# Kernel tuning notes

Hardware: AMD Instinct MI355X
Metric: run time of the kernel (lower is better)

## Reference

```python
import jax, jax.numpy as jnp
import numpy as np

BN_EPS = 1e-5

# Binary activation with hardtanh STE semantics (forward: sign)
@jax.custom_vjp
def binary_act(x):
    return jnp.sign(x)

def _ba_fwd(x):
    return jnp.sign(x), x

def _ba_bwd(x, g):
    return (jnp.where(jnp.abs(x) > 1.0, 0.0, g),)

binary_act.defvjp(_ba_fwd, _ba_bwd)

# Binary weight quantizer (forward: sign, backward: identity STE)
@jax.custom_vjp
def binary_w(x):
    return jnp.sign(x)

def _bw_fwd(x):
    return jnp.sign(x), None

def _bw_bwd(_, g):
    return (g,)

binary_w.defvjp(_bw_fwd, _bw_bwd)


def setup_inputs() -> dict:
    key = jax.random.key(0)
    k1, k2, k3 = jax.random.split(key, 3)
    B, C_in, H, W_sp = 32, 256, 56, 56
    C_out, KH, KW = 256, 3, 3
    x = jax.random.normal(k1, (B, C_in, H, W_sp), dtype=jnp.float32)
    weight = jax.random.normal(k2, (C_out, C_in, KH, KW), dtype=jnp.float32) * 0.05
    bias = jax.random.normal(k3, (C_out,), dtype=jnp.float32) * 0.01
    gamma = jnp.ones((C_out,), dtype=jnp.float32)
    beta = jnp.zeros((C_out,), dtype=jnp.float32)
    return {"x": x, "weight": weight, "bias": bias, "gamma": gamma, "beta": beta}


def reference(x, weight, bias, gamma, beta):
    # --- activation binarization (A=2): sign ---
    xb = binary_act(x)
    # --- weight binarization (W=2): mean-center over in-channel dim, clamp, sign * alpha ---
    wc = weight - jnp.mean(weight, axis=1, keepdims=True)
    wc = jnp.clip(wc, -1.0, 1.0)
    alpha = jnp.mean(jnp.abs(wc), axis=(1, 2, 3), keepdims=True)  # per-output-channel scale
    wq = binary_w(wc) * alpha
    # --- conv2d, stride 1, padding 1 ---
    y = jax.lax.conv_general_dilated(
        xb, wq, window_strides=(1, 1), padding=((1, 1), (1, 1)),
        dimension_numbers=("NCHW", "OIHW", "NCHW"))
    y = y + bias[None, :, None, None]
    # --- BatchNorm2d (training-mode batch statistics, biased variance) ---
    mu = jnp.mean(y, axis=(0, 2, 3), keepdims=True)
    var = jnp.var(y, axis=(0, 2, 3), keepdims=True)
    y = (y - mu) * jax.lax.rsqrt(var + BN_EPS)
    y = y * gamma[None, :, None, None] + beta[None, :, None, None]
    # --- last_relu=1 ---
    y = jax.nn.relu(y)
    # --- last_bin=1 (A=2 -> binary activation) ---
    y = binary_act(y)
    return y
```

## Files before the change

kernel.cpp:

```cpp
#include <hip/hip_runtime.h>

typedef unsigned long long u64;
typedef int i32x4 __attribute__((ext_vector_type(4)));
typedef int i32x16 __attribute__((ext_vector_type(16)));

#define N_SP 3136
#define C_IN 256
#define C_OUT 256
#define BATCH 32
#define NBLK 896
#define XROW 64
#define XPLANE (58 * XROW * 256)
#define XSIZE ((size_t)BATCH * XPLANE)

__global__ __launch_bounds__(256) void prep_weights(const float* __restrict__ w,
                                                    char* __restrict__ A_pack,
                                                    double* __restrict__ alpha) {
    const int o = blockIdx.x;
    const int i = threadIdx.x;
    const int lane = i & 63, wvid = i >> 6;
    __shared__ double part[4][9];
    __shared__ double part2[4];

    float wv[9];
    const float* wp = w + ((size_t)o * C_IN + i) * 9;
#pragma unroll
    for (int t = 0; t < 9; ++t) wv[t] = wp[t];

#pragma unroll
    for (int t = 0; t < 9; ++t) {
        double v = (double)wv[t];
#pragma unroll
        for (int off = 32; off > 0; off >>= 1) v += __shfl_down(v, off);
        if (lane == 0) part[wvid][t] = v;
    }
    __syncthreads();

    double asum = 0.0;
#pragma unroll
    for (int t = 0; t < 9; ++t) {
        double mean = (part[0][t] + part[1][t] + part[2][t] + part[3][t]) * (1.0 / 256.0);
        double wc = (double)wv[t] - mean;
        int idx16 = ((t * 8 + (i >> 5)) * 8 + (o >> 5)) * 64 + (((i >> 4) & 1) << 5) + (o & 31);
        A_pack[(size_t)idx16 * 16 + (i & 15)] = (char)(wc > 0.0 ? 1 : -1);
        double aw = fabs(wc);
        if (aw > 1.0) aw = 1.0;
        asum += aw;
    }
#pragma unroll
    for (int off = 32; off > 0; off >>= 1) asum += __shfl_down(asum, off);
    if (lane == 0) part2[wvid] = asum;
    __syncthreads();
    if (i == 0)
        alpha[o] = (part2[0] + part2[1] + part2[2] + part2[3]) * (1.0 / 2304.0);
}

__global__ __launch_bounds__(256) void zero_borders(char* __restrict__ xsT) {
    const int tid = blockIdx.x * 256 + threadIdx.x;
    const int b = tid / 9216;
    const int r = tid - b * 9216;
    int hp, wp, c16;
    if (r < 2048) {
        hp = (r >> 10) * 57;
        wp = (r >> 4) & 63;
        c16 = (r & 15) << 4;
    } else {
        int r2 = r - 2048;
        hp = 1 + (r2 >> 7);
        int q = r2 & 127;
        int wi = q >> 4;
        wp = (wi == 0) ? 0 : 56 + wi;
        c16 = (q & 15) << 4;
    }
    *(i32x4*)(xsT + (((size_t)(b * 58 + hp) << 6) + wp) * 256 + c16) = (i32x4){0, 0, 0, 0};
}

__global__ __launch_bounds__(256) void sign_transpose(const float* __restrict__ x,
                                                      char* __restrict__ xsT) {
    const int sp0 = blockIdx.x * 64;
    const int b = blockIdx.y;
    const int lane = threadIdx.x & 63;
    const int wv = threadIdx.x >> 6;
    __shared__ char tile[64 * 272];

    const float* xp = x + ((size_t)(b * 256 + (wv << 6))) * N_SP + sp0 + lane;
#pragma unroll
    for (int q = 0; q < 4; ++q) {
        unsigned d[4];
#pragma unroll
        for (int dd = 0; dd < 4; ++dd) {
            unsigned v = 0;
#pragma unroll
            for (int kk = 0; kk < 4; ++kk) {
                int ci_l = (q << 4) + (dd << 2) + kk;
                float xv = xp[(size_t)ci_l * N_SP];
                v |= (unsigned)(xv > 0.0f ? 0x01u : 0xFFu) << (8 * kk);
            }
            d[dd] = v;
        }
        *(i32x4*)(tile + lane * 272 + (wv << 6) + (q << 4)) =
            (i32x4){(int)d[0], (int)d[1], (int)d[2], (int)d[3]};
    }
    __syncthreads();

    const int t = threadIdx.x;
#pragma unroll
    for (int j = 0; j < 4; ++j) {
        int sp_loc = (j << 4) + (t >> 4);
        int ci0 = (t & 15) << 4;
        i32x4 v = *(const i32x4*)(tile + sp_loc * 272 + ci0);
        int spg = sp0 + sp_loc;
        int h = spg / 56, w = spg - h * 56;
        size_t dst = (((size_t)(b * 58 + h + 1) << 6) + (w + 1)) * 256 + ci0;
        *(i32x4*)(xsT + dst) = v;
    }
}

__global__ __launch_bounds__(256, 2) void conv_mfma(const char* __restrict__ xsT,
                                                    const char* __restrict__ A_pack,
                                                    float* __restrict__ out,
                                                    int2* __restrict__ partials) {
    const int tid = threadIdx.x;
    const int lane = tid & 63;
    const int wv = tid >> 6;
    const int l31 = lane & 31, l5 = lane >> 5;
    const int blk = blockIdx.x;
    const int y = blockIdx.y;
    const int b = blk / 28;
    const int h0 = (blk - b * 28) * 2;
    const int co5 = y * 4 + wv;

    __shared__ char slab[4 * 66 * 272];

    {
        const char* src = xsT + ((size_t)(b * 58 + h0) << 6) * 256;
        for (int c = tid; c < 4 * 64 * 16; c += 256) {
            int dh = c >> 10, rem = c & 1023, wp = rem >> 4, c16 = (rem & 15) << 4;
            *(i32x4*)(slab + (dh * 66 + wp) * 272 + c16) =
                *(const i32x4*)(src + (size_t)dh * (XROW * 256) + wp * 256 + c16);
        }
        if (tid < 128) {
            int dh = tid >> 5, wp = 64 + ((tid >> 4) & 1), c16 = (tid & 15) << 4;
            *(i32x4*)(slab + (dh * 66 + wp) * 272 + c16) = (i32x4){0, 0, 0, 0};
        }
    }
    __syncthreads();

    i32x16 acc[2][2] = {};

#pragma unroll
    for (int tap = 0; tap < 9; ++tap) {
        const int dh = tap / 3, dw = tap % 3;
#pragma unroll
        for (int cib = 0; cib < 8; ++cib) {
            i32x4 af = *(const i32x4*)(A_pack +
                ((size_t)(((tap * 8 + cib) * 8 + co5) * 64 + lane) << 4));
            i32x4 bf[2][2];
#pragma unroll
            for (int nh = 0; nh < 2; ++nh)
#pragma unroll
                for (int row = 0; row < 2; ++row)
                    bf[nh][row] = *(const i32x4*)(slab +
                        ((dh + row) * 66 + (nh * 32 + l31) + dw) * 272 + l5 * 16 + cib * 32);
#pragma unroll
            for (int nh = 0; nh < 2; ++nh)
#pragma unroll
                for (int row = 0; row < 2; ++row)
                    acc[nh][row] = __builtin_amdgcn_mfma_i32_32x32x32_i8(
                        af, bf[nh][row], acc[nh][row], 0, 0, 0);
        }
    }

    float* ob = out + ((size_t)(b * 256 + co5 * 32)) * N_SP + h0 * 56;
#pragma unroll
    for (int nh = 0; nh < 2; ++nh) {
        const int w = nh * 32 + l31;
        if (w < 56) {
#pragma unroll
            for (int row = 0; row < 2; ++row)
#pragma unroll
                for (int reg = 0; reg < 16; ++reg) {
                    int corow = (reg & 3) + 8 * (reg >> 2) + 4 * l5;
                    ob[(size_t)corow * N_SP + row * 56 + w] = (float)acc[nh][row][reg];
                }
        }
    }

    __syncthreads();
    int* sp_s = (int*)slab;
    int* sp_q = (int*)slab + 128;
#pragma unroll
    for (int reg = 0; reg < 16; ++reg) {
        int v00 = acc[0][0][reg], v01 = acc[0][1][reg];
        int v10 = (l31 < 24) ? acc[1][0][reg] : 0;
        int v11 = (l31 < 24) ? acc[1][1][reg] : 0;
        int s = v00 + v01 + v10 + v11;
        unsigned q = (unsigned)(v00 * v00) + (unsigned)(v01 * v01)
                   + (unsigned)(v10 * v10) + (unsigned)(v11 * v11);
#pragma unroll
        for (int off = 16; off > 0; off >>= 1) {
            s += __shfl_xor(s, off);
            q += (unsigned)__shfl_xor((int)q, off);
        }
        if (l31 == 0) {
            int corow = (reg & 3) + 8 * (reg >> 2) + 4 * l5;
            sp_s[wv * 32 + corow] = s;
            sp_q[wv * 32 + corow] = (int)q;
        }
    }
    __syncthreads();
    if (tid < 128)
        partials[(size_t)(y * 128 + tid) * NBLK + blk] = make_int2(sp_s[tid], sp_q[tid]);
}

__global__ __launch_bounds__(256) void stats_consts(const int2* __restrict__ partials,
                                                    const double* __restrict__ alpha,
                                                    const float* __restrict__ gamma,
                                                    const float* __restrict__ beta,
                                                    double* __restrict__ AB) {
    const int c = blockIdx.x;
    const int t = threadIdx.x;
    long long s1 = 0, s2 = 0;
    for (int blk = t; blk < NBLK; blk += 256) {
        int2 v = partials[(size_t)c * NBLK + blk];
        s1 += v.x;
        s2 += (long long)v.y;
    }
#pragma unroll
    for (int off = 32; off > 0; off >>= 1) {
        s1 += __shfl_down(s1, off);
        s2 += __shfl_down(s2, off);
    }
    __shared__ long long p1[4], p2[4];
    if ((t & 63) == 0) { p1[t >> 6] = s1; p2[t >> 6] = s2; }
    __syncthreads();
    if (t == 0) {
        double S1 = (double)(p1[0] + p1[1] + p1[2] + p1[3]);
        double S2 = (double)(p2[0] + p2[1] + p2[2] + p2[3]);
        const double N = (double)(BATCH * N_SP);
        double mu = S1 / N;
        double var = S2 / N - mu * mu;
        double a = alpha[c];
        double vy = a * a * var;
        double scale = (double)gamma[c] / sqrt(vy + 1e-5);
        double A = a * scale;
        double B = (double)beta[c] - A * mu;
        AB[c] = A;
        AB[C_OUT + c] = B;
    }
}

__global__ __launch_bounds__(256) void finalize(float* __restrict__ out,
                                                const double* __restrict__ AB) {
    const unsigned i4 = blockIdx.x * 256 + threadIdx.x;
    const unsigned e = i4 << 2;
    const int c = (int)((e / N_SP) & (C_OUT - 1));
    const double A = AB[c];
    const double B = AB[C_OUT + c];
    float4 v = ((float4*)out)[i4];
    v.x = (A * (double)v.x + B) > 0.0 ? 1.0f : 0.0f;
    v.y = (A * (double)v.y + B) > 0.0 ? 1.0f : 0.0f;
    v.z = (A * (double)v.z + B) > 0.0 ? 1.0f : 0.0f;
    v.w = (A * (double)v.w + B) > 0.0 ? 1.0f : 0.0f;
    ((float4*)out)[i4] = v;
}

extern "C" void kernel_launch(void* const* d_in, const int* in_sizes, int n_in,
                              void* d_out, int out_size, void* d_ws, size_t ws_size,
                              hipStream_t stream) {
    const float* x      = (const float*)d_in[0];
    const float* weight = (const float*)d_in[1];
    const float* bias   = (const float*)d_in[2];   (void)bias;
    const float* gamma  = (const float*)d_in[3];
    const float* beta   = (const float*)d_in[4];
    float* out = (float*)d_out;

    char* ws = (char*)d_ws;
    double* alpha = (double*)(ws + 4096);
    double* AB    = (double*)(ws + 8192);
    char*   A_pack = (char*)(ws + 16384);
    char*   xsT   = (char*)(ws + (1 << 20));
    int2*   partials = (int2*)(ws + 32 * (1 << 20));

    prep_weights<<<C_OUT, 256, 0, stream>>>(weight, A_pack, alpha);
    zero_borders<<<1152, 256, 0, stream>>>(xsT);
    sign_transpose<<<dim3(49, BATCH), 256, 0, stream>>>(x, xsT);
    conv_mfma<<<dim3(NBLK, 2), 256, 0, stream>>>(xsT, A_pack, out, partials);
    stats_consts<<<C_OUT, 256, 0, stream>>>(partials, alpha, gamma, beta, AB);
    finalize<<<(out_size / 4) / 256, 256, 0, stream>>>(out, AB);
}
```

Baseline: 346.9 us.

## Retile conv to one output row per block covering all output channels

```diff
diff --git a/kernel.cpp b/kernel.cpp
--- a/kernel.cpp
+++ b/kernel.cpp
@@ -8,7 +8,7 @@
 #define C_IN 256
 #define C_OUT 256
 #define BATCH 32
-#define NBLK 896
+#define NBLK 1792
 #define XROW 64
 #define XPLANE (58 * XROW * 256)
 #define XSIZE ((size_t)BATCH * XPLANE)
@@ -116,7 +116,7 @@
     }
 }
 
-__global__ __launch_bounds__(256, 2) void conv_mfma(const char* __restrict__ xsT,
+__global__ __launch_bounds__(256, 3) void conv_mfma(const char* __restrict__ xsT,
                                                     const char* __restrict__ A_pack,
                                                     float* __restrict__ out,
                                                     int2* __restrict__ partials) {
@@ -125,23 +125,19 @@
     const int wv = tid >> 6;
     const int l31 = lane & 31, l5 = lane >> 5;
     const int blk = blockIdx.x;
-    const int y = blockIdx.y;
-    const int b = blk / 28;
-    const int h0 = (blk - b * 28) * 2;
-    const int co5 = y * 4 + wv;
-
-    __shared__ char slab[4 * 66 * 272];
+    const int b = blk / 56;
+    const int h0 = blk - b * 56;
+
+    __shared__ char slab[3 * 58 * 272];
 
     {
         const char* src = xsT + ((size_t)(b * 58 + h0) << 6) * 256;
-        for (int c = tid; c < 4 * 64 * 16; c += 256) {
-            int dh = c >> 10, rem = c & 1023, wp = rem >> 4, c16 = (rem & 15) << 4;
-            *(i32x4*)(slab + (dh * 66 + wp) * 272 + c16) =
+        for (int c = tid; c < 3 * 58 * 16; c += 256) {
+            int dh = c / (58 * 16);
+            int rem = c - dh * (58 * 16);
+            int wp = rem >> 4, c16 = (rem & 15) << 4;
+            *(i32x4*)(slab + (dh * 58 + wp) * 272 + c16) =
                 *(const i32x4*)(src + (size_t)dh * (XROW * 256) + wp * 256 + c16);
-        }
-        if (tid < 128) {
-            int dh = tid >> 5, wp = 64 + ((tid >> 4) & 1), c16 = (tid & 15) << 4;
-            *(i32x4*)(slab + (dh * 66 + wp) * 272 + c16) = (i32x4){0, 0, 0, 0};
         }
     }
     __syncthreads();
@@ -151,66 +147,66 @@
 #pragma unroll
     for (int tap = 0; tap < 9; ++tap) {
         const int dh = tap / 3, dw = tap % 3;
+        const char* s0 = slab + (dh * 58 + (l31 + dw)) * 272 + l5 * 16;
+        int w1 = 32 + l31 + dw;
+        if (w1 > 57) w1 = 57;
+        const char* s1 = slab + (dh * 58 + w1) * 272 + l5 * 16;
+        const char* ap = A_pack + ((size_t)((tap * 8) * 8 + 2 * wv) * 64 + lane) * 16;
 #pragma unroll
         for (int cib = 0; cib < 8; ++cib) {
-            i32x4 af = *(const i32x4*)(A_pack +
-                ((size_t)(((tap * 8 + cib) * 8 + co5) * 64 + lane) << 4));
-            i32x4 bf[2][2];
-#pragma unroll
-            for (int nh = 0; nh < 2; ++nh)
-#pragma unroll
-                for (int row = 0; row < 2; ++row)
-                    bf[nh][row] = *(const i32x4*)(slab +
-                        ((dh + row) * 66 + (nh * 32 + l31) + dw) * 272 + l5 * 16 + cib * 32);
-#pragma unroll
-            for (int nh = 0; nh < 2; ++nh)
-#pragma unroll
-                for (int row = 0; row < 2; ++row)
-                    acc[nh][row] = __builtin_amdgcn_mfma_i32_32x32x32_i8(
-                        af, bf[nh][row], acc[nh][row], 0, 0, 0);
-        }
-    }
-
-    float* ob = out + ((size_t)(b * 256 + co5 * 32)) * N_SP + h0 * 56;
-#pragma unroll
-    for (int nh = 0; nh < 2; ++nh) {
-        const int w = nh * 32 + l31;
-        if (w < 56) {
-#pragma unroll
-            for (int row = 0; row < 2; ++row)
+            i32x4 a0 = *(const i32x4*)(ap + (size_t)cib * 8192);
+            i32x4 a1 = *(const i32x4*)(ap + (size_t)cib * 8192 + 1024);
+            i32x4 b0 = *(const i32x4*)(s0 + cib * 32);
+            i32x4 b1 = *(const i32x4*)(s1 + cib * 32);
+            acc[0][0] = __builtin_amdgcn_mfma_i32_32x32x32_i8(a0, b0, acc[0][0], 0, 0, 0);
+            acc[0][1] = __builtin_amdgcn_mfma_i32_32x32x32_i8(a0, b1, acc[0][1], 0, 0, 0);
+            acc[1][0] = __builtin_amdgcn_mfma_i32_32x32x32_i8(a1, b0, acc[1][0], 0, 0, 0);
+            acc[1][1] = __builtin_amdgcn_mfma_i32_32x32x32_i8(a1, b1, acc[1][1], 0, 0, 0);
+        }
+    }
+
+    float* ob = out + ((size_t)(b * 256)) * N_SP + h0 * 56;
+#pragma unroll
+    for (int co_i = 0; co_i < 2; ++co_i) {
+        const int co5 = 2 * wv + co_i;
+#pragma unroll
+        for (int nh = 0; nh < 2; ++nh) {
+            const int w = nh * 32 + l31;
+            if (w < 56) {
 #pragma unroll
                 for (int reg = 0; reg < 16; ++reg) {
                     int corow = (reg & 3) + 8 * (reg >> 2) + 4 * l5;
-                    ob[(size_t)corow * N_SP + row * 56 + w] = (float)acc[nh][row][reg];
+                    ob[(size_t)(co5 * 32 + corow) * N_SP + w] = (float)acc[co_i][nh][reg];
                 }
+            }
         }
     }
 
     __syncthreads();
     int* sp_s = (int*)slab;
-    int* sp_q = (int*)slab + 128;
-#pragma unroll
-    for (int reg = 0; reg < 16; ++reg) {
-        int v00 = acc[0][0][reg], v01 = acc[0][1][reg];
-        int v10 = (l31 < 24) ? acc[1][0][reg] : 0;
-        int v11 = (l31 < 24) ? acc[1][1][reg] : 0;
-        int s = v00 + v01 + v10 + v11;
-        unsigned q = (unsigned)(v00 * v00) + (unsigned)(v01 * v01)
-                   + (unsigned)(v10 * v10) + (unsigned)(v11 * v11);
-#pragma unroll
-        for (int off = 16; off > 0; off >>= 1) {
-            s += __shfl_xor(s, off);
-            q += (unsigned)__shfl_xor((int)q, off);
-        }
-        if (l31 == 0) {
-            int corow = (reg & 3) + 8 * (reg >> 2) + 4 * l5;
-            sp_s[wv * 32 + corow] = s;
-            sp_q[wv * 32 + corow] = (int)q;
-        }
-    }
-    __syncthreads();
-    if (tid < 128)
-        partials[(size_t)(y * 128 + tid) * NBLK + blk] = make_int2(sp_s[tid], sp_q[tid]);
+    int* sp_q = (int*)slab + 256;
+#pragma unroll
+    for (int co_i = 0; co_i < 2; ++co_i) {
+#pragma unroll
+        for (int reg = 0; reg < 16; ++reg) {
+            int v0 = acc[co_i][0][reg];
+            int v1 = (l31 < 24) ? acc[co_i][1][reg] : 0;
+            int s = v0 + v1;
+            unsigned q = (unsigned)(v0 * v0) + (unsigned)(v1 * v1);
+#pragma unroll
+            for (int off = 16; off > 0; off >>= 1) {
+                s += __shfl_xor(s, off);
+                q += (unsigned)__shfl_xor((int)q, off);
+            }
+            if (l31 == 0) {
+                int corow = (reg & 3) + 8 * (reg >> 2) + 4 * l5;
+                sp_s[(2 * wv + co_i) * 32 + corow] = s;
+                sp_q[(2 * wv + co_i) * 32 + corow] = (int)q;
+            }
+        }
+    }
+    __syncthreads();
+    partials[(size_t)tid * NBLK + blk] = make_int2(sp_s[tid], sp_q[tid]);
 }
 
 __global__ __launch_bounds__(256) void stats_consts(const int2* __restrict__ partials,
@@ -279,13 +275,13 @@
     double* alpha = (double*)(ws + 4096);
     double* AB    = (double*)(ws + 8192);
     char*   A_pack = (char*)(ws + 16384);
-    char*   xsT   = (char*)(ws + (1 << 20));
-    int2*   partials = (int2*)(ws + 32 * (1 << 20));
+    int2*   partials = (int2*)(ws + (1 << 20));
+    char*   xsT   = (char*)(ws + (5 << 20));
 
     prep_weights<<<C_OUT, 256, 0, stream>>>(weight, A_pack, alpha);
     zero_borders<<<1152, 256, 0, stream>>>(xsT);
     sign_transpose<<<dim3(49, BATCH), 256, 0, stream>>>(x, xsT);
-    conv_mfma<<<dim3(NBLK, 2), 256, 0, stream>>>(xsT, A_pack, out, partials);
+    conv_mfma<<<dim3(NBLK), 256, 0, stream>>>(xsT, A_pack, out, partials);
     stats_consts<<<C_OUT, 256, 0, stream>>>(partials, alpha, gamma, beta, AB);
     finalize<<<(out_size / 4) / 256, 256, 0, stream>>>(out, AB);
 }
```

Measured after the change: 322.6 us. 7.0% less time.
